# Optimization experiments

Measured on AMD Instinct MI355X. Metric: run time of the kernel, lower is better.

Reference implementation:

```python
import jax, jax.numpy as jnp
import numpy as np

B, S, HID = 2, 2048, 2048
H = 16
Q_LORA, KV_LORA = 1536, 512
D_NOPE, D_ROPE, D_V = 128, 64, 128
D_QK = D_NOPE + D_ROPE  # 192
EPS = 1e-6


def rms_norm(x, w):
    var = jnp.mean(jnp.square(x), axis=-1, keepdims=True)
    return x * jax.lax.rsqrt(var + EPS) * w


def apply_rope(x, cos, sin):
    # x: [..., d] with interleaved (real, imag) pairs; cos/sin broadcastable to [..., d//2]
    xr = x[..., 0::2]
    xi = x[..., 1::2]
    or_ = xr * cos - xi * sin
    oi_ = xr * sin + xi * cos
    return jnp.stack([or_, oi_], axis=-1).reshape(x.shape)


def setup_inputs() -> dict:
    key = jax.random.key(0)
    ks = jax.random.split(key, 8)
    std = 0.02
    x = jax.random.normal(ks[0], (B, S, HID), dtype=jnp.float32)
    # rotary frequencies (real cos/sin pair per complex freq)
    inv_freq = 1.0 / (10000.0 ** (np.arange(0, D_ROPE, 2, dtype=np.float32) / D_ROPE))
    t = np.arange(S, dtype=np.float32)
    ang = np.outer(t, inv_freq)  # [S, D_ROPE//2]
    freqs_cis = jnp.asarray(np.stack([np.cos(ang), np.sin(ang)], axis=-1))  # [S, 32, 2]
    return {
        "x": x,
        "freqs_cis": freqs_cis,
        "wq_a": std * jax.random.normal(ks[1], (Q_LORA, HID), dtype=jnp.float32),
        "q_a_norm_w": jnp.ones((Q_LORA,), dtype=jnp.float32),
        "wq_b": std * jax.random.normal(ks[2], (H * D_QK, Q_LORA), dtype=jnp.float32),
        "wkv_a": std * jax.random.normal(ks[3], (KV_LORA + D_ROPE, HID), dtype=jnp.float32),
        "kv_norm_w": jnp.ones((KV_LORA,), dtype=jnp.float32),
        "wkv_b": std * jax.random.normal(ks[4], (H * (D_NOPE + D_V), KV_LORA), dtype=jnp.float32),
        "wo": std * jax.random.normal(ks[5], (HID, H * D_V), dtype=jnp.float32),
    }


def mla_forward(x, freqs_cis, wq_a, q_a_norm_w, wq_b, wkv_a, kv_norm_w, wkv_b, wo):
    cos = freqs_cis[..., 0]  # [S, D_ROPE//2]
    sin = freqs_cis[..., 1]
    # --- queries: low-rank down, RMSNorm, up ---
    q = rms_norm(x @ wq_a.T, q_a_norm_w) @ wq_b.T          # [B,S,H*D_QK]
    q = q.reshape(B, S, H, D_QK)
    q_nope, q_pe = q[..., :D_NOPE], q[..., D_NOPE:]
    q_pe = apply_rope(q_pe, cos[None, :, None, :], sin[None, :, None, :])
    q = jnp.concatenate([q_nope, q_pe], axis=-1)           # [B,S,H,D_QK]
    # --- kv latent + shared rope key ---
    kv_all = x @ wkv_a.T                                   # [B,S,KV_LORA+D_ROPE]
    kv_lat, k_pe = kv_all[..., :KV_LORA], kv_all[..., KV_LORA:]
    k_pe = apply_rope(k_pe, cos[None, :, :], sin[None, :, :])   # [B,S,D_ROPE]
    kv = rms_norm(kv_lat, kv_norm_w) @ wkv_b.T             # [B,S,H*(D_NOPE+D_V)]
    kv = kv.reshape(B, S, H, D_NOPE + D_V)
    k_nope, v = kv[..., :D_NOPE], kv[..., D_NOPE:]
    k = jnp.concatenate(
        [k_nope, jnp.broadcast_to(k_pe[:, :, None, :], (B, S, H, D_ROPE))], axis=-1
    )                                                      # [B,S,H,D_QK]
    # --- causal softmax attention ---
    scale = D_QK ** -0.5
    scores = jnp.einsum("bqhd,bkhd->bhqk", q, k) * scale   # [B,H,S,S]
    causal = jnp.tril(jnp.ones((S, S), dtype=bool))
    scores = jnp.where(causal, scores, jnp.finfo(scores.dtype).min)
    probs = jax.nn.softmax(scores, axis=-1)
    out = jnp.einsum("bhqk,bkhd->bqhd", probs, v)          # [B,S,H,D_V]
    return out.reshape(B, S, H * D_V) @ wo.T               # [B,S,HID]


def reference(x, freqs_cis, wq_a, q_a_norm_w, wq_b, wkv_a, kv_norm_w, wkv_b, wo):
    return mla_forward(x, freqs_cis, wq_a, q_a_norm_w, wq_b, wkv_a, kv_norm_w, wkv_b, wo)
```

## Files before the change

### kernel.cpp

```cpp
#include <hip/hip_runtime.h>

typedef __bf16 bf16_t;
typedef bf16_t bf16x8 __attribute__((ext_vector_type(8)));
typedef bf16_t bf16x4v __attribute__((ext_vector_type(4)));
typedef float f32x4 __attribute__((ext_vector_type(4)));

static constexpr float QSCALE = 0.07216878364870323f * 1.44269504088896341f;

#define AS1 __attribute__((address_space(1)))
#define AS3 __attribute__((address_space(3)))
__device__ __forceinline__ void g2lds16(const void* g, void* l) {
  __builtin_amdgcn_global_load_lds((const AS1 void*)g, (AS3 void*)l, 16, 0, 0);
}

__global__ __launch_bounds__(256) void k_cast_all(
    const float* __restrict__ s0, const float* __restrict__ s1, const float* __restrict__ s2,
    const float* __restrict__ s3, const float* __restrict__ s4, const float* __restrict__ s5,
    bf16_t* __restrict__ d0, bf16_t* __restrict__ d1, bf16_t* __restrict__ d2,
    bf16_t* __restrict__ d3, bf16_t* __restrict__ d4, bf16_t* __restrict__ d5,
    int c1, int c2, int c3, int c4, int c5, int c6) {
  int g = blockIdx.x * 256 + threadIdx.x;
  const float* s; bf16_t* d; int off;
  if (g < c1) { s = s0; d = d0; off = 0; }
  else if (g < c2) { s = s1; d = d1; off = c1; }
  else if (g < c3) { s = s2; d = d2; off = c2; }
  else if (g < c4) { s = s3; d = d3; off = c3; }
  else if (g < c5) { s = s4; d = d4; off = c4; }
  else if (g < c6) { s = s5; d = d5; off = c5; }
  else return;
  int i = g - off;
  const float4* p = (const float4*)s + (size_t)i * 2;
  float4 a = p[0], b = p[1];
  bf16x8 o = {(bf16_t)a.x, (bf16_t)a.y, (bf16_t)a.z, (bf16_t)a.w,
              (bf16_t)b.x, (bf16_t)b.y, (bf16_t)b.z, (bf16_t)b.w};
  ((bf16x8*)d)[i] = o;
}

template <int MODE>
__global__ __launch_bounds__(256) void k_gemm_t(
    const bf16_t* __restrict__ A, const bf16_t* __restrict__ Bt,
    void* __restrict__ Cout, int M, int N, int K, const float* __restrict__ freqs,
    bf16_t* __restrict__ aux) {
  __shared__ __align__(16) bf16_t As[128][32];
  __shared__ __align__(16) bf16_t Bs[128][32];
  const int tid = threadIdx.x;
  const int lane = tid & 63, wid = tid >> 6;
  const int wr = wid >> 1, wc = wid & 1;
  const int lr = lane & 15, lk = lane >> 4;
  const int bm = blockIdx.y * 128, bn = blockIdx.x * 128;
  f32x4 acc[4][4] = {};
  const int srow = wid * 16 + (lane >> 2);
  const int scol = (lane & 3) * 8;
  const bf16_t* a0 = A + (size_t)(bm + srow) * K + scol;
  const bf16_t* a1 = A + (size_t)(bm + 64 + srow) * K + scol;
  const bf16_t* b0 = Bt + (size_t)(bn + srow) * K + scol;
  const bf16_t* b1 = Bt + (size_t)(bn + 64 + srow) * K + scol;
  bf16_t* lA0 = &As[wid * 16][0];
  bf16_t* lA1 = &As[64 + wid * 16][0];
  bf16_t* lB0 = &Bs[wid * 16][0];
  bf16_t* lB1 = &Bs[64 + wid * 16][0];
  for (int kt = 0; kt < K; kt += 32) {
    g2lds16(a0 + kt, lA0);
    g2lds16(a1 + kt, lA1);
    g2lds16(b0 + kt, lB0);
    g2lds16(b1 + kt, lB1);
    __syncthreads();
    bf16x8 af[4], bff[4];
#pragma unroll
    for (int i = 0; i < 4; i++)
      af[i] = *(const bf16x8*)(&As[wr * 64 + i * 16 + lr][lk * 8]);
#pragma unroll
    for (int j = 0; j < 4; j++)
      bff[j] = *(const bf16x8*)(&Bs[wc * 64 + j * 16 + lr][lk * 8]);
#pragma unroll
    for (int i = 0; i < 4; i++)
#pragma unroll
      for (int j = 0; j < 4; j++)
        acc[i][j] = __builtin_amdgcn_mfma_f32_16x16x32_bf16(af[i], bff[j], acc[i][j], 0, 0, 0);
    __syncthreads();
  }
  const int crow = bm + wr * 64 + lk * 4;
  const int ccol = bn + wc * 64 + lr;
#pragma unroll
  for (int i = 0; i < 4; i++)
#pragma unroll
    for (int j = 0; j < 4; j++) {
      int col = ccol + j * 16;
      if (col < N) {
        if constexpr (MODE == 0) {
          float* C = (float*)Cout;
#pragma unroll
          for (int r = 0; r < 4; r++)
            C[(size_t)(crow + i * 16 + r) * N + col] = acc[i][j][r];
        } else if constexpr (MODE == 1) {
          bf16_t* C = (bf16_t*)Cout;
#pragma unroll
          for (int r = 0; r < 4; r++)
            C[(size_t)(crow + i * 16 + r) * N + col] = (bf16_t)acc[i][j][r];
        } else if constexpr (MODE == 2) {
          bf16_t* Qd = (bf16_t*)Cout;
          int hcol = col / 192;
          int dmod = col - hcol * 192;
#pragma unroll
          for (int r = 0; r < 4; r++) {
            int row = crow + i * 16 + r;
            int bb = row >> 11, s = row & 2047;
            float v = acc[i][j][r];
            float partner = __shfl_xor(v, 1);
            if (dmod >= 128) {
              int pbase = ((lr & 1) == 0) ? (dmod - 128) : (dmod - 129);
              int p = pbase >> 1;
              float c = freqs[s * 64 + 2 * p];
              float sn = freqs[s * 64 + 2 * p + 1];
              v = ((lr & 1) == 0) ? (v * c - partner * sn) : (partner * sn + v * c);
            }
            Qd[((size_t)(bb * 16 + hcol) * 2048 + s) * 192 + dmod] = (bf16_t)(v * QSCALE);
          }
        } else {
          int h = bn >> 8;
          int d = col & 127;
          if ((bn & 128) == 0) {
#pragma unroll
            for (int r = 0; r < 4; r++) {
              int row = crow + i * 16 + r;
              int bb = row >> 11, s = row & 2047;
              aux[((size_t)(bb * 16 + h) * 2048 + s) * 192 + d] = (bf16_t)acc[i][j][r];
            }
          } else {
            bf16_t* C = (bf16_t*)Cout;
#pragma unroll
            for (int r = 0; r < 4; r++)
              C[(size_t)(crow + i * 16 + r) * 2048 + h * 128 + d] = (bf16_t)acc[i][j][r];
          }
        }
      }
    }
}

__global__ __launch_bounds__(256) void k_rms_q(const bf16_t* __restrict__ in,
                                               const float* __restrict__ w,
                                               bf16_t* __restrict__ out) {
  int row = blockIdx.x, tid = threadIdx.x;
  const bf16x8* x8 = (const bf16x8*)(in + (size_t)row * 2112);
  float ss = 0.f;
  bf16x8 v = {};
  if (tid < 192) {
    v = x8[tid];
#pragma unroll
    for (int j = 0; j < 8; j++) { float f = (float)v[j]; ss += f * f; }
  }
  for (int m = 32; m; m >>= 1) ss += __shfl_xor(ss, m);
  __shared__ float parts[4];
  if ((tid & 63) == 0) parts[tid >> 6] = ss;
  __syncthreads();
  float inv = rsqrtf((parts[0] + parts[1] + parts[2] + parts[3]) * (1.f / 1536.f) + 1e-6f);
  if (tid < 192) {
    const float4* w4 = (const float4*)(w + tid * 8);
    float4 w0 = w4[0], w1 = w4[1];
    bf16x8 o = {(bf16_t)((float)v[0] * inv * w0.x), (bf16_t)((float)v[1] * inv * w0.y),
                (bf16_t)((float)v[2] * inv * w0.z), (bf16_t)((float)v[3] * inv * w0.w),
                (bf16_t)((float)v[4] * inv * w1.x), (bf16_t)((float)v[5] * inv * w1.y),
                (bf16_t)((float)v[6] * inv * w1.z), (bf16_t)((float)v[7] * inv * w1.w)};
    *(bf16x8*)(out + (size_t)row * 1536 + tid * 8) = o;
  }
}

__global__ __launch_bounds__(256) void k_kv_norm_rope(const bf16_t* __restrict__ qkva,
                                                      const float* __restrict__ w,
                                                      const float* __restrict__ freqs,
                                                      bf16_t* __restrict__ kvn,
                                                      bf16_t* __restrict__ Kf) {
  int row = blockIdx.x, tid = threadIdx.x;
  int b = row >> 11, s = row & 2047;
  const bf16_t* x = qkva + (size_t)row * 2112 + 1536;
  float ss = 0.f;
  float vf[4] = {0.f, 0.f, 0.f, 0.f};
  if (tid < 128) {
    bf16x4v v4 = *(const bf16x4v*)(x + tid * 4);
#pragma unroll
    for (int j = 0; j < 4; j++) { vf[j] = (float)v4[j]; ss += vf[j] * vf[j]; }
  }
  for (int m = 32; m; m >>= 1) ss += __shfl_xor(ss, m);
  __shared__ float parts[4];
  if ((tid & 63) == 0) parts[tid >> 6] = ss;
  __syncthreads();
  float inv = rsqrtf((parts[0] + parts[1] + parts[2] + parts[3]) * (1.f / 512.f) + 1e-6f);
  if (tid < 128) {
    float4 ww = ((const float4*)w)[tid];
    bf16x4v o = {(bf16_t)(vf[0] * inv * ww.x), (bf16_t)(vf[1] * inv * ww.y),
                 (bf16_t)(vf[2] * inv * ww.z), (bf16_t)(vf[3] * inv * ww.w)};
    *(bf16x4v*)(kvn + (size_t)row * 512 + tid * 4) = o;
  }
  if (tid < 32) {
    float xr = (float)x[512 + 2 * tid], xi = (float)x[513 + 2 * tid];
    float c = freqs[s * 64 + 2 * tid], sn = freqs[s * 64 + 2 * tid + 1];
    bf16_t o0 = (bf16_t)(xr * c - xi * sn);
    bf16_t o1 = (bf16_t)(xr * sn + xi * c);
#pragma unroll
    for (int h = 0; h < 16; h++) {
      size_t base = ((size_t)(b * 16 + h) * 2048 + s) * 192 + 128 + 2 * tid;
      Kf[base] = o0;
      Kf[base + 1] = o1;
    }
  }
}

__global__ __launch_bounds__(256) void k_split_v(const bf16_t* __restrict__ Vc,
                                                 bf16_t* __restrict__ Vt) {
  __shared__ bf16_t vt_l[128][66];
  int s0 = blockIdx.x * 64;
  int h = blockIdx.y;
#pragma unroll 4
  for (int i = 0; i < 32; i++) {
    int idx = i * 256 + threadIdx.x;
    int r = idx >> 7, d = idx & 127;
    vt_l[d][r] = Vc[(size_t)(s0 + r) * 2048 + h * 128 + d];
  }
  __syncthreads();
#pragma unroll 4
  for (int i = 0; i < 32; i++) {
    int idx = i * 256 + threadIdx.x;
    int d = idx >> 6, ss = idx & 63;
    int row = s0 + ss;
    int b = row >> 11, s = row & 2047;
    Vt[((size_t)(b * 16 + h) * 128 + d) * 2048 + s] = vt_l[d][ss];
  }
}

__global__ __launch_bounds__(512) void k_attn(const bf16_t* __restrict__ Q,
                                              const bf16_t* __restrict__ Kf,
                                              const bf16_t* __restrict__ Vt,
                                              bf16_t* __restrict__ O) {
  __shared__ __align__(16) bf16_t Ks[2][3][64][64];
  __shared__ __align__(16) bf16_t Vs[2][128][64];
  __shared__ __align__(16) bf16_t P[8][16][64];
  const int tid = threadIdx.x;
  const int lane = tid & 63, wid = tid >> 6;
  const int lr = lane & 15, lk = lane >> 4;
  const int r8 = lane >> 3, c8 = lane & 7;
  const int qt = (int)gridDim.x - 1 - (int)blockIdx.x;
  const int qb = qt * 128;
  const int qbw = qb + wid * 16;
  const int bh = blockIdx.y;
  const int b = bh >> 4, h = bh & 15;
  const bf16_t* Qp = Q + (size_t)bh * 2048 * 192;
  const bf16_t* Kb = Kf + (size_t)bh * 2048 * 192;
  const bf16_t* Vb = Vt + (size_t)bh * 128 * 2048;
  bf16x8 bq[6];
#pragma unroll
  for (int f = 0; f < 6; f++)
    bq[f] = *(const bf16x8*)(Qp + (size_t)(qbw + lr) * 192 + f * 32 + lk * 8);
  f32x4 acc[8] = {};
  float m_s = -1e30f, l_s = 0.f;
  const int q_mine = qbw + lr;
  auto stage = [&](int buf, int k0) {
#pragma unroll
    for (int t = 0; t < 3; t++) {
      int i = wid * 3 + t;
      int p = i >> 3, rb = i & 7;
      int row = rb * 8 + r8;
      g2lds16(Kb + (size_t)(k0 + row) * 192 + p * 64 + ((c8 ^ (row & 7)) * 8),
              &Ks[buf][p][row][c8 * 8]);
    }
#pragma unroll
    for (int t = 0; t < 2; t++) {
      int i = wid * 2 + t;
      int d = i * 8 + r8;
      g2lds16(Vb + (size_t)d * 2048 + k0 + ((c8 ^ (d & 7)) * 8), &Vs[buf][d][c8 * 8]);
    }
  };
  const int nkt = qt * 2 + 2;
  stage(0, 0);
  __syncthreads();
  int buf = 0;
  for (int kt = 0; kt < nkt; kt++) {
    const int k0 = kt * 64;
    if (kt + 1 < nkt) stage(buf ^ 1, k0 + 64);
    if (k0 <= qbw + 15) {
      f32x4 sc[4];
#pragma unroll
      for (int hh = 0; hh < 4; hh++) {
        f32x4 a = {};
        const int row = hh * 16 + lr;
#pragma unroll
        for (int f = 0; f < 6; f++) {
          const int cc = (f & 1) * 4 + lk;
          bf16x8 ak = *(const bf16x8*)(&Ks[buf][f >> 1][row][((cc ^ (row & 7)) & 7) * 8]);
          a = __builtin_amdgcn_mfma_f32_16x16x32_bf16(ak, bq[f], a, 0, 0, 0);
        }
        sc[hh] = a;
      }
      if (k0 + 63 > qbw) {
#pragma unroll
        for (int hh = 0; hh < 4; hh++) {
          int key = k0 + hh * 16 + lk * 4;
#pragma unroll
          for (int r = 0; r < 4; r++)
            if (key + r > q_mine) sc[hh][r] = -1e30f;
        }
      }
      float t0 = fmaxf(fmaxf(sc[0][0], sc[0][1]), fmaxf(sc[0][2], sc[0][3]));
      float t1 = fmaxf(fmaxf(sc[1][0], sc[1][1]), fmaxf(sc[1][2], sc[1][3]));
      float t2 = fmaxf(fmaxf(sc[2][0], sc[2][1]), fmaxf(sc[2][2], sc[2][3]));
      float t3 = fmaxf(fmaxf(sc[3][0], sc[3][1]), fmaxf(sc[3][2], sc[3][3]));
      float tmax = fmaxf(fmaxf(t0, t1), fmaxf(t2, t3));
      tmax = fmaxf(tmax, __shfl_xor(tmax, 16));
      tmax = fmaxf(tmax, __shfl_xor(tmax, 32));
      float mn = fmaxf(m_s, tmax);
      float alpha = exp2f(m_s - mn);
      m_s = mn;
      float sm = 0.f;
#pragma unroll
      for (int hh = 0; hh < 4; hh++) {
#pragma unroll
        for (int r = 0; r < 4; r++) {
          float p = exp2f(sc[hh][r] - mn);
          sc[hh][r] = p;
          sm += p;
        }
      }
      sm += __shfl_xor(sm, 16);
      sm += __shfl_xor(sm, 32);
      l_s = l_s * alpha + sm;
#pragma unroll
      for (int hh = 0; hh < 4; hh++) {
        int c = hh * 2 + (lk >> 1);
        int coff = ((c ^ (lr & 7)) * 8) + (lk & 1) * 4;
        bf16x4v pv = {(bf16_t)sc[hh][0], (bf16_t)sc[hh][1], (bf16_t)sc[hh][2], (bf16_t)sc[hh][3]};
        *(bf16x4v*)(&P[wid][lr][coff]) = pv;
      }
      float ab[4];
#pragma unroll
      for (int r = 0; r < 4; r++) ab[r] = __shfl(alpha, lk * 4 + r);
#pragma unroll
      for (int j = 0; j < 8; j++)
#pragma unroll
        for (int r = 0; r < 4; r++) acc[j][r] *= ab[r];
#pragma unroll
      for (int s2 = 0; s2 < 2; s2++) {
        bf16x8 pa = *(const bf16x8*)(&P[wid][lr][((s2 * 4 + lk) ^ (lr & 7)) * 8]);
#pragma unroll
        for (int j = 0; j < 8; j++) {
          const int d = j * 16 + lr;
          bf16x8 bv = *(const bf16x8*)(&Vs[buf][d][((s2 * 4 + lk) ^ (d & 7)) * 8]);
          acc[j] = __builtin_amdgcn_mfma_f32_16x16x32_bf16(pa, bv, acc[j], 0, 0, 0);
        }
      }
    }
    __syncthreads();
    buf ^= 1;
  }
  float linv = 1.f / l_s;
  float lb[4];
#pragma unroll
  for (int r = 0; r < 4; r++) lb[r] = __shfl(linv, lk * 4 + r);
  size_t orow = (size_t)b * 2048 + qbw + lk * 4;
#pragma unroll
  for (int j = 0; j < 8; j++)
#pragma unroll
    for (int r = 0; r < 4; r++)
      O[(orow + r) * 2048 + h * 128 + j * 16 + lr] = (bf16_t)(acc[j][r] * lb[r]);
}

extern "C" void kernel_launch(void* const* d_in, const int* in_sizes, int n_in,
                              void* d_out, int out_size, void* d_ws, size_t ws_size,
                              hipStream_t stream) {
  const float* x = (const float*)d_in[0];
  const float* freqs = (const float*)d_in[1];
  const float* wq_a = (const float*)d_in[2];
  const float* q_norm_w = (const float*)d_in[3];
  const float* wq_b = (const float*)d_in[4];
  const float* wkv_a = (const float*)d_in[5];
  const float* kv_norm_w = (const float*)d_in[6];
  const float* wkv_b = (const float*)d_in[7];
  const float* wo = (const float*)d_in[8];
  float* out = (float*)d_out;
  char* ws = (char*)d_ws;

  bf16_t* qkvab = (bf16_t*)(ws);
  bf16_t* Vc = (bf16_t*)(ws + 25165824);
  bf16_t* xbf = (bf16_t*)(ws + 67108864);
  bf16_t* wqab = (bf16_t*)(ws + 83886080);
  bf16_t* wkvab = (bf16_t*)(ws + 90177536);
  bf16_t* wqbb = (bf16_t*)(ws + 92536832);
  bf16_t* wkvbb = (bf16_t*)(ws + 101974016);
  bf16_t* wob = (bf16_t*)(ws + 106168320);
  bf16_t* qan = (bf16_t*)(ws + 114556928);
  bf16_t* kvn = (bf16_t*)(ws + 127139840);
  bf16_t* Qb = (bf16_t*)(ws + 131334144);
  bf16_t* Kb = (bf16_t*)(ws + 156499968);
  bf16_t* Vtb = (bf16_t*)(ws + 181665792);
  bf16_t* aob = (bf16_t*)(ws + 198443008);
  (void)in_sizes; (void)n_in; (void)out_size; (void)ws_size;

  {
    int n_x = 1048576, n_qa = 393216, n_kva = 147456, n_qb = 589824, n_kvb = 262144, n_o = 524288;
    int c1 = n_x, c2 = c1 + n_qa, c3 = c2 + n_kva, c4 = c3 + n_qb, c5 = c4 + n_kvb, c6 = c5 + n_o;
    k_cast_all<<<(c6 + 255) / 256, 256, 0, stream>>>(
        x, wq_a, wkv_a, wq_b, wkv_b, wo,
        xbf, wqab, wkvab, wqbb, wkvbb, wob,
        c1, c2, c3, c4, c5, c6);
  }

  k_gemm_t<1><<<dim3(17, 32), 256, 0, stream>>>(xbf, wqab, qkvab, 4096, 2112, 2048, nullptr, nullptr);
  k_kv_norm_rope<<<4096, 256, 0, stream>>>(qkvab, kv_norm_w, freqs, kvn, Kb);
  k_gemm_t<3><<<dim3(32, 32), 256, 0, stream>>>(kvn, wkvbb, Vc, 4096, 4096, 512, nullptr, Kb);
  k_split_v<<<dim3(64, 16), 256, 0, stream>>>(Vc, Vtb);
  k_rms_q<<<4096, 256, 0, stream>>>(qkvab, q_norm_w, qan);
  k_gemm_t<2><<<dim3(24, 32), 256, 0, stream>>>(qan, wqbb, Qb, 4096, 3072, 1536, freqs, nullptr);
  k_attn<<<dim3(16, 32), 512, 0, stream>>>(Qb, Kb, Vtb, aob);
  k_gemm_t<0><<<dim3(16, 32), 256, 0, stream>>>(aob, wob, out, 4096, 2048, 2048, nullptr, nullptr);
}
```

Before: 527.9 us.

## Rewrite attention with 32x32 MFMA, register-resident P, and lazy rescaling

The attention kernel moves from 16x16x32 to 32x32x16 bf16 MFMA tiles, with 4 waves of 32 query rows each instead of 8 waves of 16. The softmax probabilities are packed to bf16 and exchanged between lanes with shuffles instead of going through an LDS scratch buffer. The running-max rescale of the accumulator is skipped whenever the new tile max stays within 8 (log2 units) of the current max. These changes aim to cut LDS traffic, MFMA instruction count and per-tile rescale work, at the cost of more registers per thread and fewer threads to stage each K/V tile.

Result: faster. 489.5 us (-7.3%).

```diff
diff --git a/kernel.cpp b/kernel.cpp
--- a/kernel.cpp
+++ b/kernel.cpp
@@ -4,6 +4,8 @@
 typedef bf16_t bf16x8 __attribute__((ext_vector_type(8)));
 typedef bf16_t bf16x4v __attribute__((ext_vector_type(4)));
 typedef float f32x4 __attribute__((ext_vector_type(4)));
+typedef float f32x16 __attribute__((ext_vector_type(16)));
+typedef unsigned int u32;
 
 static constexpr float QSCALE = 0.07216878364870323f * 1.44269504088896341f;
 
@@ -11,6 +13,12 @@
 #define AS3 __attribute__((address_space(3)))
 __device__ __forceinline__ void g2lds16(const void* g, void* l) {
   __builtin_amdgcn_global_load_lds((const AS1 void*)g, (AS3 void*)l, 16, 0, 0);
+}
+
+__device__ __forceinline__ u32 pack2(float a, float b) {
+  union { bf16_t h[2]; u32 u; } c;
+  c.h[0] = (bf16_t)a; c.h[1] = (bf16_t)b;
+  return c.u;
 }
 
 __global__ __launch_bounds__(256) void k_cast_all(
@@ -227,46 +235,44 @@
   }
 }
 
-__global__ __launch_bounds__(512) void k_attn(const bf16_t* __restrict__ Q,
-                                              const bf16_t* __restrict__ Kf,
-                                              const bf16_t* __restrict__ Vt,
-                                              bf16_t* __restrict__ O) {
+__global__ __launch_bounds__(256, 2) void k_attn(const bf16_t* __restrict__ Q,
+                                                 const bf16_t* __restrict__ Kf,
+                                                 const bf16_t* __restrict__ Vt,
+                                                 bf16_t* __restrict__ O) {
   __shared__ __align__(16) bf16_t Ks[2][3][64][64];
   __shared__ __align__(16) bf16_t Vs[2][128][64];
-  __shared__ __align__(16) bf16_t P[8][16][64];
   const int tid = threadIdx.x;
   const int lane = tid & 63, wid = tid >> 6;
-  const int lr = lane & 15, lk = lane >> 4;
+  const int l31 = lane & 31, hi = lane >> 5;
   const int r8 = lane >> 3, c8 = lane & 7;
   const int qt = (int)gridDim.x - 1 - (int)blockIdx.x;
   const int qb = qt * 128;
-  const int qbw = qb + wid * 16;
+  const int qbw = qb + wid * 32;
   const int bh = blockIdx.y;
   const int b = bh >> 4, h = bh & 15;
   const bf16_t* Qp = Q + (size_t)bh * 2048 * 192;
   const bf16_t* Kb = Kf + (size_t)bh * 2048 * 192;
   const bf16_t* Vb = Vt + (size_t)bh * 128 * 2048;
-  bf16x8 bq[6];
-#pragma unroll
-  for (int f = 0; f < 6; f++)
-    bq[f] = *(const bf16x8*)(Qp + (size_t)(qbw + lr) * 192 + f * 32 + lk * 8);
-  f32x4 acc[8] = {};
+  const int q_mine = qbw + l31;
+  bf16x8 bq[12];
+#pragma unroll
+  for (int kk = 0; kk < 12; kk++)
+    bq[kk] = *(const bf16x8*)(Qp + (size_t)q_mine * 192 + kk * 16 + hi * 8);
+  f32x16 acc[4] = {};
   float m_s = -1e30f, l_s = 0.f;
-  const int q_mine = qbw + lr;
   auto stage = [&](int buf, int k0) {
 #pragma unroll
-    for (int t = 0; t < 3; t++) {
-      int i = wid * 3 + t;
-      int p = i >> 3, rb = i & 7;
-      int row = rb * 8 + r8;
-      g2lds16(Kb + (size_t)(k0 + row) * 192 + p * 64 + ((c8 ^ (row & 7)) * 8),
-              &Ks[buf][p][row][c8 * 8]);
-    }
-#pragma unroll
-    for (int t = 0; t < 2; t++) {
-      int i = wid * 2 + t;
-      int d = i * 8 + r8;
-      g2lds16(Vb + (size_t)d * 2048 + k0 + ((c8 ^ (d & 7)) * 8), &Vs[buf][d][c8 * 8]);
+    for (int t = 0; t < 10; t++) {
+      int i = t * 4 + wid;
+      if (i < 24) {
+        int p = i >> 3, rb = i & 7;
+        int row = rb * 8 + r8;
+        g2lds16(Kb + (size_t)(k0 + row) * 192 + p * 64 + ((c8 ^ (row & 7)) * 8),
+                &Ks[buf][p][row][c8 * 8]);
+      } else {
+        int d = (i - 24) * 8 + r8;
+        g2lds16(Vb + (size_t)d * 2048 + k0 + ((c8 ^ (d & 7)) * 8), &Vs[buf][d][c8 * 8]);
+      }
     }
   };
   const int nkt = qt * 2 + 2;
@@ -276,74 +282,79 @@
   for (int kt = 0; kt < nkt; kt++) {
     const int k0 = kt * 64;
     if (kt + 1 < nkt) stage(buf ^ 1, k0 + 64);
-    if (k0 <= qbw + 15) {
-      f32x4 sc[4];
-#pragma unroll
-      for (int hh = 0; hh < 4; hh++) {
-        f32x4 a = {};
-        const int row = hh * 16 + lr;
-#pragma unroll
-        for (int f = 0; f < 6; f++) {
-          const int cc = (f & 1) * 4 + lk;
-          bf16x8 ak = *(const bf16x8*)(&Ks[buf][f >> 1][row][((cc ^ (row & 7)) & 7) * 8]);
-          a = __builtin_amdgcn_mfma_f32_16x16x32_bf16(ak, bq[f], a, 0, 0, 0);
+    if (k0 <= qbw + 31) {
+      f32x16 sg0 = {}, sg1 = {};
+      const int rk0 = l31, rk1 = 32 + l31;
+#pragma unroll
+      for (int kk = 0; kk < 12; kk++) {
+        int c = kk * 2 + hi;
+        int p = c >> 3, cip = c & 7;
+        bf16x8 ak0 = *(const bf16x8*)(&Ks[buf][p][rk0][(cip ^ (rk0 & 7)) * 8]);
+        sg0 = __builtin_amdgcn_mfma_f32_32x32x16_bf16(ak0, bq[kk], sg0, 0, 0, 0);
+        bf16x8 ak1 = *(const bf16x8*)(&Ks[buf][p][rk1][(cip ^ (rk1 & 7)) * 8]);
+        sg1 = __builtin_amdgcn_mfma_f32_32x32x16_bf16(ak1, bq[kk], sg1, 0, 0, 0);
+      }
+      if (k0 + 63 > qbw) {
+#pragma unroll
+        for (int r = 0; r < 16; r++) {
+          int ko = (r & 3) + 8 * (r >> 2) + 4 * hi;
+          if (k0 + ko > q_mine) sg0[r] = -1e30f;
+          if (k0 + 32 + ko > q_mine) sg1[r] = -1e30f;
         }
-        sc[hh] = a;
-      }
-      if (k0 + 63 > qbw) {
-#pragma unroll
-        for (int hh = 0; hh < 4; hh++) {
-          int key = k0 + hh * 16 + lk * 4;
-#pragma unroll
-          for (int r = 0; r < 4; r++)
-            if (key + r > q_mine) sc[hh][r] = -1e30f;
+      }
+      float tmax = -1e30f;
+#pragma unroll
+      for (int r = 0; r < 16; r++) tmax = fmaxf(tmax, fmaxf(sg0[r], sg1[r]));
+      tmax = fmaxf(tmax, __shfl_xor(tmax, 32));
+      bool defer = __all(tmax <= m_s + 8.0f);
+      float mn = defer ? m_s : fmaxf(m_s, tmax);
+      if (!defer) {
+        float alpha = exp2f(m_s - mn);
+        m_s = mn;
+        l_s *= alpha;
+#pragma unroll
+        for (int jb = 0; jb < 4; jb++)
+#pragma unroll
+          for (int r = 0; r < 16; r++) acc[jb][r] *= alpha;
+      }
+      float sm = 0.f;
+#pragma unroll
+      for (int r = 0; r < 16; r++) {
+        sg0[r] = exp2f(sg0[r] - mn);
+        sg1[r] = exp2f(sg1[r] - mn);
+        sm += sg0[r] + sg1[r];
+      }
+      sm += __shfl_xor(sm, 32);
+      l_s += sm;
+      u32 pk0[8], pk1[8], pp0[8], pp1[8];
+#pragma unroll
+      for (int i = 0; i < 8; i++) {
+        pk0[i] = pack2(sg0[2 * i], sg0[2 * i + 1]);
+        pk1[i] = pack2(sg1[2 * i], sg1[2 * i + 1]);
+        pp0[i] = __shfl_xor(pk0[i], 32);
+        pp1[i] = __shfl_xor(pk1[i], 32);
+      }
+#pragma unroll
+      for (int s = 0; s < 4; s++) {
+        const int par = s & 1;
+        union { u32 u[4]; bf16x8 v; } fr;
+        if (s < 2) {
+          fr.u[0] = hi ? pp0[4 * par + 2] : pk0[4 * par + 0];
+          fr.u[1] = hi ? pp0[4 * par + 3] : pk0[4 * par + 1];
+          fr.u[2] = hi ? pk0[4 * par + 2] : pp0[4 * par + 0];
+          fr.u[3] = hi ? pk0[4 * par + 3] : pp0[4 * par + 1];
+        } else {
+          fr.u[0] = hi ? pp1[4 * par + 2] : pk1[4 * par + 0];
+          fr.u[1] = hi ? pp1[4 * par + 3] : pk1[4 * par + 1];
+          fr.u[2] = hi ? pk1[4 * par + 2] : pp1[4 * par + 0];
+          fr.u[3] = hi ? pk1[4 * par + 3] : pp1[4 * par + 1];
         }
-      }
-      float t0 = fmaxf(fmaxf(sc[0][0], sc[0][1]), fmaxf(sc[0][2], sc[0][3]));
-      float t1 = fmaxf(fmaxf(sc[1][0], sc[1][1]), fmaxf(sc[1][2], sc[1][3]));
-      float t2 = fmaxf(fmaxf(sc[2][0], sc[2][1]), fmaxf(sc[2][2], sc[2][3]));
-      float t3 = fmaxf(fmaxf(sc[3][0], sc[3][1]), fmaxf(sc[3][2], sc[3][3]));
-      float tmax = fmaxf(fmaxf(t0, t1), fmaxf(t2, t3));
-      tmax = fmaxf(tmax, __shfl_xor(tmax, 16));
-      tmax = fmaxf(tmax, __shfl_xor(tmax, 32));
-      float mn = fmaxf(m_s, tmax);
-      float alpha = exp2f(m_s - mn);
-      m_s = mn;
-      float sm = 0.f;
-#pragma unroll
-      for (int hh = 0; hh < 4; hh++) {
-#pragma unroll
-        for (int r = 0; r < 4; r++) {
-          float p = exp2f(sc[hh][r] - mn);
-          sc[hh][r] = p;
-          sm += p;
-        }
-      }
-      sm += __shfl_xor(sm, 16);
-      sm += __shfl_xor(sm, 32);
-      l_s = l_s * alpha + sm;
-#pragma unroll
-      for (int hh = 0; hh < 4; hh++) {
-        int c = hh * 2 + (lk >> 1);
-        int coff = ((c ^ (lr & 7)) * 8) + (lk & 1) * 4;
-        bf16x4v pv = {(bf16_t)sc[hh][0], (bf16_t)sc[hh][1], (bf16_t)sc[hh][2], (bf16_t)sc[hh][3]};
-        *(bf16x4v*)(&P[wid][lr][coff]) = pv;
-      }
-      float ab[4];
-#pragma unroll
-      for (int r = 0; r < 4; r++) ab[r] = __shfl(alpha, lk * 4 + r);
-#pragma unroll
-      for (int j = 0; j < 8; j++)
-#pragma unroll
-        for (int r = 0; r < 4; r++) acc[j][r] *= ab[r];
-#pragma unroll
-      for (int s2 = 0; s2 < 2; s2++) {
-        bf16x8 pa = *(const bf16x8*)(&P[wid][lr][((s2 * 4 + lk) ^ (lr & 7)) * 8]);
-#pragma unroll
-        for (int j = 0; j < 8; j++) {
-          const int d = j * 16 + lr;
-          bf16x8 bv = *(const bf16x8*)(&Vs[buf][d][((s2 * 4 + lk) ^ (d & 7)) * 8]);
-          acc[j] = __builtin_amdgcn_mfma_f32_16x16x32_bf16(pa, bv, acc[j], 0, 0, 0);
+        const int c = s * 2 + hi;
+#pragma unroll
+        for (int jb = 0; jb < 4; jb++) {
+          const int d = jb * 32 + l31;
+          bf16x8 av = *(const bf16x8*)(&Vs[buf][d][((c ^ (d & 7)) & 7) * 8]);
+          acc[jb] = __builtin_amdgcn_mfma_f32_32x32x16_bf16(av, fr.v, acc[jb], 0, 0, 0);
         }
       }
     }
@@ -351,15 +362,16 @@
     buf ^= 1;
   }
   float linv = 1.f / l_s;
-  float lb[4];
-#pragma unroll
-  for (int r = 0; r < 4; r++) lb[r] = __shfl(linv, lk * 4 + r);
-  size_t orow = (size_t)b * 2048 + qbw + lk * 4;
-#pragma unroll
-  for (int j = 0; j < 8; j++)
-#pragma unroll
-    for (int r = 0; r < 4; r++)
-      O[(orow + r) * 2048 + h * 128 + j * 16 + lr] = (bf16_t)(acc[j][r] * lb[r]);
+  bf16_t* orow = O + ((size_t)b * 2048 + q_mine) * 2048 + h * 128;
+#pragma unroll
+  for (int jb = 0; jb < 4; jb++)
+#pragma unroll
+    for (int k = 0; k < 4; k++) {
+      int d0 = jb * 32 + 8 * k + 4 * hi;
+      bf16x4v ov = {(bf16_t)(acc[jb][4 * k] * linv), (bf16_t)(acc[jb][4 * k + 1] * linv),
+                    (bf16_t)(acc[jb][4 * k + 2] * linv), (bf16_t)(acc[jb][4 * k + 3] * linv)};
+      *(bf16x4v*)(orow + d0) = ov;
+    }
 }
 
 extern "C" void kernel_launch(void* const* d_in, const int* in_sizes, int n_in,
@@ -408,6 +420,6 @@
   k_split_v<<<dim3(64, 16), 256, 0, stream>>>(Vc, Vtb);
   k_rms_q<<<4096, 256, 0, stream>>>(qkvab, q_norm_w, qan);
   k_gemm_t<2><<<dim3(24, 32), 256, 0, stream>>>(qan, wqbb, Qb, 4096, 3072, 1536, freqs, nullptr);
-  k_attn<<<dim3(16, 32), 512, 0, stream>>>(Qb, Kb, Vtb, aob);
+  k_attn<<<dim3(16, 32), 256, 0, stream>>>(Qb, Kb, Vtb, aob);
   k_gemm_t<0><<<dim3(16, 32), 256, 0, stream>>>(aob, wob, out, 4096, 2048, 2048, nullptr, nullptr);
 }
```
